# Kernel tuning notes

Hardware: AMD Instinct MI355X
Metric: run time of the kernel (lower is better)

## Reference

```python
import jax, jax.numpy as jnp
import numpy as np

N = 100000   # nodes
E = 600000   # edges
G = 512      # graphs in batch
EPS = 1e-5   # LayerNorm eps
IN_DIM = 60 + 2 + 12  # dyn feats*frames + dims + st embedding
H = 128


def setup_inputs() -> dict:
    key = jax.random.key(0)
    ks = jax.random.split(key, 32)
    inp = {
        "x": jax.random.normal(ks[0], (N, 60), jnp.float32),
        "xdims": jax.random.uniform(ks[1], (N, 2), jnp.float32),
        "xsttype": jax.random.randint(ks[2], (N,), 0, 256, jnp.int32),
        "edge_index": jax.random.randint(ks[3], (2, E), 0, N, jnp.int32),
        "batch": jnp.sort(jax.random.randint(ks[4], (N,), 0, G, jnp.int32)),
        "emb": jax.random.normal(ks[5], (256, 12), jnp.float32),
    }
    def lin(k, i, o):
        s = 1.0 / np.sqrt(i)
        return jax.random.uniform(k, (i, o), jnp.float32, -s, s)
    dims = [IN_DIM, H, H]
    for l in range(2):
        i, o = dims[l], dims[l + 1]
        inp[f"Wl{l}"] = lin(ks[6 + 4 * l], i, o)   # lin_l: applied to aggregated neighbors
        inp[f"bl{l}"] = jnp.zeros((o,), jnp.float32)
        inp[f"Wr{l}"] = lin(ks[7 + 4 * l], i, o)   # lin_r: applied to root (no bias, PyG SAGEConv)
        inp[f"g{l}"] = jnp.ones((o,), jnp.float32)   # LayerNorm gamma
        inp[f"bn{l}"] = jnp.zeros((o,), jnp.float32)  # LayerNorm beta
    ld = [2 * H, 50, 50, 10]
    for l in range(3):
        inp[f"Wf{l}"] = lin(ks[20 + l], ld[l], ld[l + 1])
        inp[f"bf{l}"] = jnp.zeros((ld[l + 1],), jnp.float32)
    return inp


def _layer_norm(h, g, b):
    mu = jnp.mean(h, axis=-1, keepdims=True)
    var = jnp.mean(jnp.square(h - mu), axis=-1, keepdims=True)
    return (h - mu) * jax.lax.rsqrt(var + EPS) * g + b


def reference(x, xdims, xsttype, edge_index, batch, emb,
              Wl0, bl0, Wr0, g0, bn0,
              Wl1, bl1, Wr1, g1, bn1,
              Wf0, bf0, Wf1, bf1, Wf2, bf2):
    # node feature assembly: [N, 60+2+12]
    h = jnp.concatenate([x, xdims, emb[xsttype]], axis=1)

    src, dst = edge_index[0], edge_index[1]
    deg = jax.ops.segment_sum(jnp.ones((E,), h.dtype), dst, num_segments=N)
    inv_deg = (1.0 / jnp.maximum(deg, 1.0))[:, None]

    for Wl, bl, Wr, g, bn in ((Wl0, bl0, Wr0, g0, bn0), (Wl1, bl1, Wr1, g1, bn1)):
        # SAGEConv (mean aggr): out = lin_l(mean_j x_j) + lin_r(x_i)
        agg = jax.ops.segment_sum(h[src], dst, num_segments=N) * inv_deg
        h = agg @ Wl + bl + h @ Wr
        h = jax.nn.relu(_layer_norm(h, g, bn))  # dropout inactive (eval)

    # global mean / max pooling over graphs
    cnt = jax.ops.segment_sum(jnp.ones((N,), h.dtype), batch, num_segments=G)
    xmean = jax.ops.segment_sum(h, batch, num_segments=G) / jnp.maximum(cnt, 1.0)[:, None]
    xmax = jax.ops.segment_max(h, batch, num_segments=G)
    z = jnp.concatenate([xmean, xmax], axis=1)  # [G, 2H]

    for Wf, bf in ((Wf0, bf0), (Wf1, bf1), (Wf2, bf2)):
        z = jax.nn.relu(z @ Wf + bf)  # Linear + ReLU + Dropout(eval)
    return z
```

## Files before the change

kernel.cpp:

```cpp
#include <hip/hip_runtime.h>

#define NN 100000
#define NP 100096
#define NT (NP / 32)
#define EE 600000
#define GG 512
#define LN_EPS 1e-5f

typedef __attribute__((ext_vector_type(8))) __bf16 bf16x8;
typedef __attribute__((ext_vector_type(4))) float f32x4;

__device__ __forceinline__ unsigned short f2bf(float f) {
    unsigned int u = __float_as_uint(f);
    u = (u + 0x7fffu + ((u >> 16) & 1u)) >> 16;
    return (unsigned short)u;
}
__device__ __forceinline__ unsigned int pack2(float a, float b) {
    return (unsigned int)f2bf(a) | ((unsigned int)f2bf(b) << 16);
}
__device__ __forceinline__ void acc8(float* s, uint4 v) {
    s[0] += __uint_as_float(v.x << 16);
    s[1] += __uint_as_float(v.x & 0xffff0000u);
    s[2] += __uint_as_float(v.y << 16);
    s[3] += __uint_as_float(v.y & 0xffff0000u);
    s[4] += __uint_as_float(v.z << 16);
    s[5] += __uint_as_float(v.z & 0xffff0000u);
    s[6] += __uint_as_float(v.w << 16);
    s[7] += __uint_as_float(v.w & 0xffff0000u);
}

#define PREP_A (NP * 10)
#define PREP_W0 (128 * 160)
#define PREP_W1 (128 * 256)
#define PREP_TOT (PREP_A + PREP_W0 + PREP_W1 + EE)

__global__ __launch_bounds__(256) void prep_kernel(
    const float* __restrict__ x, const float* __restrict__ xdims,
    const int* __restrict__ stt, const float* __restrict__ emb,
    const int* __restrict__ ei,
    const float* __restrict__ Wl0, const float* __restrict__ Wr0,
    const float* __restrict__ Wl1, const float* __restrict__ Wr1,
    unsigned short* __restrict__ H0r,
    unsigned short* __restrict__ Wt0, unsigned short* __restrict__ Wt1,
    int* __restrict__ deg)
{
    int idx = blockIdx.x * 256 + threadIdx.x;
    if (idx < PREP_A) {
        int node = idx / 10;
        int c8 = (idx - node * 10) * 8;
        unsigned short vals[8];
        if (node < NN) {
            int st = stt[node];
            #pragma unroll
            for (int i = 0; i < 8; ++i) {
                int f = c8 + i;
                float v = 0.f;
                if (f < 60)      v = x[node * 60 + f];
                else if (f < 62) v = xdims[node * 2 + (f - 60)];
                else if (f < 74) v = emb[st * 12 + (f - 62)];
                vals[i] = f2bf(v);
            }
        } else {
            #pragma unroll
            for (int i = 0; i < 8; ++i) vals[i] = 0;
        }
        uint4 o;
        o.x = (unsigned)vals[0] | ((unsigned)vals[1] << 16);
        o.y = (unsigned)vals[2] | ((unsigned)vals[3] << 16);
        o.z = (unsigned)vals[4] | ((unsigned)vals[5] << 16);
        o.w = (unsigned)vals[6] | ((unsigned)vals[7] << 16);
        *(uint4*)(H0r + (size_t)node * 80 + c8) = o;
    } else if (idx < PREP_A + PREP_W0) {
        int j = idx - PREP_A;
        int n = j / 160, k = j - n * 160;
        float v = 0.f;
        if (k < 74)                  v = Wl0[k * 128 + n];
        else if (k >= 80 && k < 154) v = Wr0[(k - 80) * 128 + n];
        Wt0[(size_t)n * 160 + k] = f2bf(v);
    } else if (idx < PREP_A + PREP_W0 + PREP_W1) {
        int j = idx - PREP_A - PREP_W0;
        int n = j >> 8, k = j & 255;
        float v = (k < 128) ? Wl1[k * 128 + n] : Wr1[(k - 128) * 128 + n];
        Wt1[(size_t)n * 256 + k] = f2bf(v);
    } else if (idx < PREP_TOT) {
        int e = idx - PREP_A - PREP_W0 - PREP_W1;
        atomicAdd(&deg[ei[EE + e]], 1);
    }
}

__global__ __launch_bounds__(256) void scan1_kernel(
    const int* __restrict__ deg, int* __restrict__ offs, int* __restrict__ bsum)
{
    __shared__ int ts[256];
    int t = threadIdx.x;
    int base = blockIdx.x * 2048 + t * 8;
    int d[8];
    if (base + 8 <= NN) {
        int4 a = *(const int4*)&deg[base];
        int4 b = *(const int4*)&deg[base + 4];
        d[0]=a.x; d[1]=a.y; d[2]=a.z; d[3]=a.w;
        d[4]=b.x; d[5]=b.y; d[6]=b.z; d[7]=b.w;
    } else {
        #pragma unroll
        for (int i = 0; i < 8; ++i) d[i] = (base + i < NN) ? deg[base + i] : 0;
    }
    int e[8]; int run = 0;
    #pragma unroll
    for (int i = 0; i < 8; ++i) { e[i] = run; run += d[i]; }
    ts[t] = run;
    int tot = run;
    __syncthreads();
    for (int off = 1; off < 256; off <<= 1) {
        int u = (t >= off) ? ts[t - off] : 0;
        __syncthreads();
        ts[t] += u;
        __syncthreads();
    }
    int pre = ts[t] - tot;
    #pragma unroll
    for (int i = 0; i < 8; ++i) if (base + i < NN) offs[base + i] = e[i] + pre;
    if (t == 255) bsum[blockIdx.x] = ts[255];
}

__global__ void scan2_kernel(int* __restrict__ bsum, int nb)
{
    int t = threadIdx.x;
    int v = (t < nb) ? bsum[t] : 0;
    int inc = v;
    for (int off = 1; off < 64; off <<= 1) {
        int u = __shfl_up(inc, off, 64);
        if (t >= off) inc += u;
    }
    if (t < nb) bsum[t] = inc - v;
}

__global__ __launch_bounds__(256) void fill_csr_kernel(
    const int* __restrict__ ei, int* __restrict__ cur,
    const int* __restrict__ offs, const int* __restrict__ bsum,
    int* __restrict__ csr)
{
    int e = blockIdx.x * 256 + threadIdx.x;
    if (e >= EE) return;
    int d = ei[EE + e];
    int p = offs[d] + bsum[d >> 11] + atomicAdd(&cur[d], 1);
    csr[p] = ei[e];
}

template<int K, bool POOL>
__global__ __launch_bounds__(256, 4) void gemm_kernel(
    const unsigned short* __restrict__ Hr,
    const unsigned short* __restrict__ Wt,
    const float* __restrict__ bias, const float* __restrict__ gamma,
    const float* __restrict__ beta,
    unsigned short* __restrict__ outH,
    const int* __restrict__ batch,
    float* __restrict__ psum, int* __restrict__ pmax, int* __restrict__ gcnt,
    const int* __restrict__ csr, const int* __restrict__ offs,
    const int* __restrict__ bsum, const int* __restrict__ deg)
{
    constexpr int KT = K / 32, AS = K + 8, KH = K / 2, CH = KH / 8;
    constexpr int SMEM = (32 * AS * 2 > 32 * 128 * 4) ? 32 * AS * 2 : 32 * 128 * 4;
    __shared__ __align__(16) char smem[SMEM];
    unsigned short* Asm = (unsigned short*)smem;
    float* Hs = (float*)smem;
    __shared__ __align__(16) float sP[32 * 4];
    __shared__ __align__(16) float qP[32 * 4];
    __shared__ int bS[POOL ? 32 : 1];

    const int tid = threadIdx.x;
    const int n0 = blockIdx.x * 32;
    const int l = tid & 63, w = tid >> 6;
    const int fg = l >> 4, c0 = l & 15;

    if (POOL && tid < 32) {
        int gn = n0 + tid;
        bS[tid] = (gn < NN) ? batch[gn] : -1;
    }
    float bia[2], gam[2], bet[2];
    #pragma unroll
    for (int j = 0; j < 2; ++j) {
        int col = (2 * w + j) * 16 + c0;
        bia[j] = bias[col]; gam[j] = gamma[col]; bet[j] = beta[col];
    }
    const unsigned short* bp0 = Wt + (size_t)((2 * w + 0) * 16 + c0) * K + fg * 8;
    const unsigned short* bp1 = Wt + (size_t)((2 * w + 1) * 16 + c0) * K + fg * 8;

    {
        const int ln = tid & 15, nl = tid >> 4;
        #pragma unroll
        for (int half = 0; half < 2; ++half) {
            int node = half * 16 + nl;
            int gn = n0 + node;
            if (ln < CH) {
                uint4 rv = *(const uint4*)(Hr + (size_t)gn * KH + ln * 8);
                int d = 0, st = 0;
                if (gn < NN) { d = deg[gn]; st = offs[gn] + bsum[gn >> 11]; }
                float iv = 1.0f / (float)(d > 1 ? d : 1);
                float s[8];
                #pragma unroll
                for (int i = 0; i < 8; ++i) s[i] = 0.f;
                int e = 0;
                for (; e + 4 <= d; e += 4) {
                    int i0 = csr[st + e],     i1 = csr[st + e + 1];
                    int i2 = csr[st + e + 2], i3 = csr[st + e + 3];
                    uint4 v0 = *(const uint4*)(Hr + (size_t)i0 * KH + ln * 8);
                    uint4 v1 = *(const uint4*)(Hr + (size_t)i1 * KH + ln * 8);
                    uint4 v2 = *(const uint4*)(Hr + (size_t)i2 * KH + ln * 8);
                    uint4 v3 = *(const uint4*)(Hr + (size_t)i3 * KH + ln * 8);
                    acc8(s, v0); acc8(s, v1); acc8(s, v2); acc8(s, v3);
                }
                for (; e < d; ++e) {
                    int i0 = csr[st + e];
                    uint4 v0 = *(const uint4*)(Hr + (size_t)i0 * KH + ln * 8);
                    acc8(s, v0);
                }
                uint4 o;
                o.x = pack2(s[0] * iv, s[1] * iv);
                o.y = pack2(s[2] * iv, s[3] * iv);
                o.z = pack2(s[4] * iv, s[5] * iv);
                o.w = pack2(s[6] * iv, s[7] * iv);
                *(uint4*)(Asm + node * AS + ln * 8) = o;
                *(uint4*)(Asm + node * AS + KH + ln * 8) = rv;
            }
        }
    }

    const unsigned short* ar0 = Asm + (0 * 16 + c0) * AS + fg * 8;
    const unsigned short* ar1 = Asm + (1 * 16 + c0) * AS + fg * 8;
    __syncthreads();

    f32x4 acc[2][2];
    acc[0][0] = (f32x4){0.f,0.f,0.f,0.f}; acc[0][1] = (f32x4){0.f,0.f,0.f,0.f};
    acc[1][0] = (f32x4){0.f,0.f,0.f,0.f}; acc[1][1] = (f32x4){0.f,0.f,0.f,0.f};

    #pragma unroll
    for (int kt = 0; kt < KT; ++kt) {
        bf16x8 b0 = *(const bf16x8*)(bp0 + kt * 32);
        bf16x8 b1 = *(const bf16x8*)(bp1 + kt * 32);
        bf16x8 a0 = *(const bf16x8*)(ar0 + kt * 32);
        bf16x8 a1 = *(const bf16x8*)(ar1 + kt * 32);
        acc[0][0] = __builtin_amdgcn_mfma_f32_16x16x32_bf16(a0, b0, acc[0][0], 0, 0, 0);
        acc[0][1] = __builtin_amdgcn_mfma_f32_16x16x32_bf16(a0, b1, acc[0][1], 0, 0, 0);
        acc[1][0] = __builtin_amdgcn_mfma_f32_16x16x32_bf16(a1, b0, acc[1][0], 0, 0, 0);
        acc[1][1] = __builtin_amdgcn_mfma_f32_16x16x32_bf16(a1, b1, acc[1][1], 0, 0, 0);
    }

    #pragma unroll
    for (int m = 0; m < 2; ++m) {
        #pragma unroll
        for (int r = 0; r < 4; ++r) {
            float h0v = acc[m][0][r] + bia[0];
            float h1v = acc[m][1][r] + bia[1];
            float s = h0v + h1v, q = h0v * h0v + h1v * h1v;
            #pragma unroll
            for (int mm = 1; mm < 16; mm <<= 1) {
                s += __shfl_xor(s, mm, 64);
                q += __shfl_xor(q, mm, 64);
            }
            if (c0 == 0) {
                int node = m * 16 + fg * 4 + r;
                sP[node * 4 + w] = s;
                qP[node * 4 + w] = q;
            }
        }
    }
    __syncthreads();

    #pragma unroll
    for (int m = 0; m < 2; ++m) {
        #pragma unroll
        for (int r = 0; r < 4; ++r) {
            int node = m * 16 + fg * 4 + r;
            float4 sv = *(const float4*)&sP[node * 4];
            float4 qv = *(const float4*)&qP[node * 4];
            float s = (sv.x + sv.y) + (sv.z + sv.w);
            float q = (qv.x + qv.y) + (qv.z + qv.w);
            float mu   = s * (1.f / 128.f);
            float var  = q * (1.f / 128.f) - mu * mu;
            float rinv = rsqrtf(var + LN_EPS);
            float h0v = acc[m][0][r] + bia[0];
            float h1v = acc[m][1][r] + bia[1];
            float v0 = fmaxf(0.f, (h0v - mu) * rinv * gam[0] + bet[0]);
            float v1 = fmaxf(0.f, (h1v - mu) * rinv * gam[1] + bet[1]);
            if (POOL) {
                Hs[node * 128 + (2 * w) * 16 + c0]     = v0;
                Hs[node * 128 + (2 * w + 1) * 16 + c0] = v1;
            } else {
                size_t gn = (size_t)(n0 + node);
                outH[gn * 128 + (2 * w) * 16 + c0]     = f2bf(v0);
                outH[gn * 128 + (2 * w + 1) * 16 + c0] = f2bf(v1);
            }
        }
    }
    if (!POOL) return;
    __syncthreads();

    if (tid < 128) {
        int j = tid;
        int curg = -1; float s = 0.f, m = 0.f; int rl = 0;
        #pragma unroll 4
        for (int n = 0; n < 32; ++n) {
            int gb = bS[n];
            if (gb < 0) break;
            if (gb != curg) {
                if (curg >= 0) {
                    atomicAdd(&psum[curg * 128 + j], s);
                    atomicMax(&pmax[curg * 128 + j], __float_as_int(m));
                    if (j == 0) atomicAdd(&gcnt[curg], rl);
                }
                curg = gb; s = 0.f; m = 0.f; rl = 0;
            }
            float v = Hs[n * 128 + j];
            s += v; m = fmaxf(m, v);
            rl += 1;
        }
        if (curg >= 0) {
            atomicAdd(&psum[curg * 128 + j], s);
            atomicMax(&pmax[curg * 128 + j], __float_as_int(m));
            if (j == 0) atomicAdd(&gcnt[curg], rl);
        }
    }
}

__global__ __launch_bounds__(64) void mlp_kernel(
    const float* __restrict__ psum, const int* __restrict__ pmax,
    const int* __restrict__ gcnt,
    const float* __restrict__ Wf0, const float* __restrict__ bf0,
    const float* __restrict__ Wf1, const float* __restrict__ bf1,
    const float* __restrict__ Wf2, const float* __restrict__ bf2,
    float* __restrict__ out)
{
    __shared__ float z[256];
    __shared__ float t1[50];
    __shared__ float t2[50];
    int g = blockIdx.x, t = threadIdx.x;
    int c = gcnt[g];
    float ic = 1.0f / (float)(c > 1 ? c : 1);
    for (int j = t; j < 128; j += 64) {
        z[j]       = psum[g * 128 + j] * ic;
        z[128 + j] = __int_as_float(pmax[g * 128 + j]);
    }
    __syncthreads();
    if (t < 50) {
        float a = bf0[t];
        for (int k = 0; k < 256; ++k) a = fmaf(z[k], Wf0[k * 50 + t], a);
        t1[t] = fmaxf(a, 0.0f);
    }
    __syncthreads();
    if (t < 50) {
        float a = bf1[t];
        for (int k = 0; k < 50; ++k) a = fmaf(t1[k], Wf1[k * 50 + t], a);
        t2[t] = fmaxf(a, 0.0f);
    }
    __syncthreads();
    if (t < 10) {
        float a = bf2[t];
        for (int k = 0; k < 50; ++k) a = fmaf(t2[k], Wf2[k * 10 + t], a);
        out[g * 10 + t] = fmaxf(a, 0.0f);
    }
}

extern "C" void kernel_launch(void* const* d_in, const int* in_sizes, int n_in,
                              void* d_out, int out_size, void* d_ws, size_t ws_size,
                              hipStream_t stream)
{
    const float* x     = (const float*)d_in[0];
    const float* xdims = (const float*)d_in[1];
    const int*   stt   = (const int*)d_in[2];
    const int*   ei    = (const int*)d_in[3];
    const int*   batch = (const int*)d_in[4];
    const float* emb   = (const float*)d_in[5];
    const float* Wl0   = (const float*)d_in[6];
    const float* bl0   = (const float*)d_in[7];
    const float* Wr0   = (const float*)d_in[8];
    const float* g0    = (const float*)d_in[9];
    const float* bn0   = (const float*)d_in[10];
    const float* Wl1   = (const float*)d_in[11];
    const float* bl1   = (const float*)d_in[12];
    const float* Wr1   = (const float*)d_in[13];
    const float* g1    = (const float*)d_in[14];
    const float* bn1   = (const float*)d_in[15];
    const float* Wf0   = (const float*)d_in[16];
    const float* bf0   = (const float*)d_in[17];
    const float* Wf1   = (const float*)d_in[18];
    const float* bf1   = (const float*)d_in[19];
    const float* Wf2   = (const float*)d_in[20];
    const float* bf2   = (const float*)d_in[21];

    char* w = (char*)d_ws;
    unsigned short* H0r = (unsigned short*)w; w += (size_t)NP * 80 * 2;
    unsigned short* H1  = (unsigned short*)w; w += (size_t)NP * 128 * 2;
    unsigned short* Wt0 = (unsigned short*)w; w += (size_t)128 * 160 * 2;
    unsigned short* Wt1 = (unsigned short*)w; w += (size_t)128 * 256 * 2;
    int*   csr    = (int*)w;   w += (size_t)EE * 4;
    int*   offs   = (int*)w;   w += (size_t)NN * 4;
    int*   bsum   = (int*)w;   w += 1024;
    char* zbeg = w;
    int*   deg  = (int*)w;   w += (size_t)NP * 4;
    int*   cur  = (int*)w;   w += (size_t)NN * 4;
    float* psum = (float*)w; w += (size_t)GG * 128 * 4;
    int*   pmax = (int*)w;   w += (size_t)GG * 128 * 4;
    int*   gcnt = (int*)w;   w += (size_t)GG * 4;
    size_t zsz = (size_t)(w - zbeg);

    hipMemsetAsync(zbeg, 0, zsz, stream);

    prep_kernel<<<(PREP_TOT + 255) / 256, 256, 0, stream>>>(
        x, xdims, stt, emb, ei, Wl0, Wr0, Wl1, Wr1, H0r, Wt0, Wt1, deg);

    int nb = (NN + 2047) / 2048;
    scan1_kernel<<<nb, 256, 0, stream>>>(deg, offs, bsum);
    scan2_kernel<<<1, 64, 0, stream>>>(bsum, nb);
    fill_csr_kernel<<<(EE + 255) / 256, 256, 0, stream>>>(ei, cur, offs, bsum, csr);

    gemm_kernel<160, false><<<NT, 256, 0, stream>>>(
        H0r, Wt0, bl0, g0, bn0, H1, nullptr, nullptr, nullptr, nullptr,
        csr, offs, bsum, deg);
    gemm_kernel<256, true><<<NT, 256, 0, stream>>>(
        H1, Wt1, bl1, g1, bn1, nullptr, batch, psum, pmax, gcnt,
        csr, offs, bsum, deg);

    mlp_kernel<<<GG, 64, 0, stream>>>(psum, pmax, gcnt, Wf0, bf0, Wf1, bf1, Wf2, bf2,
                                      (float*)d_out);
}
```

Baseline: 283.5 us.

## Use 512-thread blocks so each thread gathers one node and computes one column tile

The fused aggregate+GEMM+LayerNorm kernel moves from 256 to 512 threads per 32-node block. Each thread now gathers one node's neighbors instead of two, and each wave owns one 16-column tile instead of two. The LayerNorm partial sums grow to 8 waves per node, and padded rows are written as zeros in layer 1. The intent is more parallelism and memory-level concurrency in the latency-bound neighbor gather, at the cost of fewer MFMAs per wave and more cross-wave reduction. The MLP kernel also gets multiple independent accumulators to break FMA dependency chains.

```diff
diff --git a/kernel.cpp b/kernel.cpp
--- a/kernel.cpp
+++ b/kernel.cpp
@@ -147,7 +147,7 @@
 }
 
 template<int K, bool POOL>
-__global__ __launch_bounds__(256, 4) void gemm_kernel(
+__global__ __launch_bounds__(512, 2) void gemm_kernel(
     const unsigned short* __restrict__ Hr,
     const unsigned short* __restrict__ Wt,
     const float* __restrict__ bias, const float* __restrict__ gamma,
@@ -163,8 +163,8 @@
     __shared__ __align__(16) char smem[SMEM];
     unsigned short* Asm = (unsigned short*)smem;
     float* Hs = (float*)smem;
-    __shared__ __align__(16) float sP[32 * 4];
-    __shared__ __align__(16) float qP[32 * 4];
+    __shared__ __align__(16) float sP[32 * 8];
+    __shared__ __align__(16) float qP[32 * 8];
     __shared__ int bS[POOL ? 32 : 1];
 
     const int tid = threadIdx.x;
@@ -176,82 +176,69 @@
         int gn = n0 + tid;
         bS[tid] = (gn < NN) ? batch[gn] : -1;
     }
-    float bia[2], gam[2], bet[2];
-    #pragma unroll
-    for (int j = 0; j < 2; ++j) {
-        int col = (2 * w + j) * 16 + c0;
-        bia[j] = bias[col]; gam[j] = gamma[col]; bet[j] = beta[col];
-    }
-    const unsigned short* bp0 = Wt + (size_t)((2 * w + 0) * 16 + c0) * K + fg * 8;
-    const unsigned short* bp1 = Wt + (size_t)((2 * w + 1) * 16 + c0) * K + fg * 8;
 
     {
         const int ln = tid & 15, nl = tid >> 4;
-        #pragma unroll
-        for (int half = 0; half < 2; ++half) {
-            int node = half * 16 + nl;
-            int gn = n0 + node;
-            if (ln < CH) {
-                uint4 rv = *(const uint4*)(Hr + (size_t)gn * KH + ln * 8);
-                int d = 0, st = 0;
-                if (gn < NN) { d = deg[gn]; st = offs[gn] + bsum[gn >> 11]; }
-                float iv = 1.0f / (float)(d > 1 ? d : 1);
-                float s[8];
-                #pragma unroll
-                for (int i = 0; i < 8; ++i) s[i] = 0.f;
-                int e = 0;
-                for (; e + 4 <= d; e += 4) {
-                    int i0 = csr[st + e],     i1 = csr[st + e + 1];
-                    int i2 = csr[st + e + 2], i3 = csr[st + e + 3];
-                    uint4 v0 = *(const uint4*)(Hr + (size_t)i0 * KH + ln * 8);
-                    uint4 v1 = *(const uint4*)(Hr + (size_t)i1 * KH + ln * 8);
-                    uint4 v2 = *(const uint4*)(Hr + (size_t)i2 * KH + ln * 8);
-                    uint4 v3 = *(const uint4*)(Hr + (size_t)i3 * KH + ln * 8);
-                    acc8(s, v0); acc8(s, v1); acc8(s, v2); acc8(s, v3);
-                }
-                for (; e < d; ++e) {
-                    int i0 = csr[st + e];
-                    uint4 v0 = *(const uint4*)(Hr + (size_t)i0 * KH + ln * 8);
-                    acc8(s, v0);
-                }
-                uint4 o;
-                o.x = pack2(s[0] * iv, s[1] * iv);
-                o.y = pack2(s[2] * iv, s[3] * iv);
-                o.z = pack2(s[4] * iv, s[5] * iv);
-                o.w = pack2(s[6] * iv, s[7] * iv);
-                *(uint4*)(Asm + node * AS + ln * 8) = o;
-                *(uint4*)(Asm + node * AS + KH + ln * 8) = rv;
-            }
-        }
-    }
-
+        int gn = n0 + nl;
+        if (ln < CH) {
+            uint4 rv = *(const uint4*)(Hr + (size_t)gn * KH + ln * 8);
+            int d = 0, st = 0;
+            if (gn < NN) { d = deg[gn]; st = offs[gn] + bsum[gn >> 11]; }
+            float iv = 1.0f / (float)(d > 1 ? d : 1);
+            float s[8];
+            #pragma unroll
+            for (int i = 0; i < 8; ++i) s[i] = 0.f;
+            int e = 0;
+            for (; e + 4 <= d; e += 4) {
+                int i0 = csr[st + e],     i1 = csr[st + e + 1];
+                int i2 = csr[st + e + 2], i3 = csr[st + e + 3];
+                uint4 v0 = *(const uint4*)(Hr + (size_t)i0 * KH + ln * 8);
+                uint4 v1 = *(const uint4*)(Hr + (size_t)i1 * KH + ln * 8);
+                uint4 v2 = *(const uint4*)(Hr + (size_t)i2 * KH + ln * 8);
+                uint4 v3 = *(const uint4*)(Hr + (size_t)i3 * KH + ln * 8);
+                acc8(s, v0); acc8(s, v1); acc8(s, v2); acc8(s, v3);
+            }
+            for (; e < d; ++e) {
+                int i0 = csr[st + e];
+                uint4 v0 = *(const uint4*)(Hr + (size_t)i0 * KH + ln * 8);
+                acc8(s, v0);
+            }
+            uint4 o;
+            o.x = pack2(s[0] * iv, s[1] * iv);
+            o.y = pack2(s[2] * iv, s[3] * iv);
+            o.z = pack2(s[4] * iv, s[5] * iv);
+            o.w = pack2(s[6] * iv, s[7] * iv);
+            *(uint4*)(Asm + nl * AS + ln * 8) = o;
+            *(uint4*)(Asm + nl * AS + KH + ln * 8) = rv;
+        }
+    }
+
+    const int col = w * 16 + c0;
+    const unsigned short* bp = Wt + (size_t)col * K + fg * 8;
     const unsigned short* ar0 = Asm + (0 * 16 + c0) * AS + fg * 8;
     const unsigned short* ar1 = Asm + (1 * 16 + c0) * AS + fg * 8;
-    __syncthreads();
-
-    f32x4 acc[2][2];
-    acc[0][0] = (f32x4){0.f,0.f,0.f,0.f}; acc[0][1] = (f32x4){0.f,0.f,0.f,0.f};
-    acc[1][0] = (f32x4){0.f,0.f,0.f,0.f}; acc[1][1] = (f32x4){0.f,0.f,0.f,0.f};
+    float bia = bias[col], gam = gamma[col], bet = beta[col];
+    __syncthreads();
+
+    f32x4 acc[2];
+    acc[0] = (f32x4){0.f,0.f,0.f,0.f};
+    acc[1] = (f32x4){0.f,0.f,0.f,0.f};
 
     #pragma unroll
     for (int kt = 0; kt < KT; ++kt) {
-        bf16x8 b0 = *(const bf16x8*)(bp0 + kt * 32);
-        bf16x8 b1 = *(const bf16x8*)(bp1 + kt * 32);
+        bf16x8 b  = *(const bf16x8*)(bp  + kt * 32);
         bf16x8 a0 = *(const bf16x8*)(ar0 + kt * 32);
         bf16x8 a1 = *(const bf16x8*)(ar1 + kt * 32);
-        acc[0][0] = __builtin_amdgcn_mfma_f32_16x16x32_bf16(a0, b0, acc[0][0], 0, 0, 0);
-        acc[0][1] = __builtin_amdgcn_mfma_f32_16x16x32_bf16(a0, b1, acc[0][1], 0, 0, 0);
-        acc[1][0] = __builtin_amdgcn_mfma_f32_16x16x32_bf16(a1, b0, acc[1][0], 0, 0, 0);
-        acc[1][1] = __builtin_amdgcn_mfma_f32_16x16x32_bf16(a1, b1, acc[1][1], 0, 0, 0);
+        acc[0] = __builtin_amdgcn_mfma_f32_16x16x32_bf16(a0, b, acc[0], 0, 0, 0);
+        acc[1] = __builtin_amdgcn_mfma_f32_16x16x32_bf16(a1, b, acc[1], 0, 0, 0);
     }
 
     #pragma unroll
     for (int m = 0; m < 2; ++m) {
         #pragma unroll
         for (int r = 0; r < 4; ++r) {
-            float h0v = acc[m][0][r] + bia[0];
-            float h1v = acc[m][1][r] + bia[1];
-            float s = h0v + h1v, q = h0v * h0v + h1v * h1v;
+            float hv = acc[m][r] + bia;
+            float s = hv, q = hv * hv;
             #pragma unroll
             for (int mm = 1; mm < 16; mm <<= 1) {
                 s += __shfl_xor(s, mm, 64);
@@ -259,8 +246,8 @@
             }
             if (c0 == 0) {
                 int node = m * 16 + fg * 4 + r;
-                sP[node * 4 + w] = s;
-                qP[node * 4 + w] = q;
+                sP[node * 8 + w] = s;
+                qP[node * 8 + w] = q;
             }
         }
     }
@@ -271,24 +258,23 @@
         #pragma unroll
         for (int r = 0; r < 4; ++r) {
             int node = m * 16 + fg * 4 + r;
-            float4 sv = *(const float4*)&sP[node * 4];
-            float4 qv = *(const float4*)&qP[node * 4];
-            float s = (sv.x + sv.y) + (sv.z + sv.w);
-            float q = (qv.x + qv.y) + (qv.z + qv.w);
+            float4 sa = *(const float4*)&sP[node * 8];
+            float4 sb = *(const float4*)&sP[node * 8 + 4];
+            float4 qa = *(const float4*)&qP[node * 8];
+            float4 qb = *(const float4*)&qP[node * 8 + 4];
+            float s = ((sa.x + sa.y) + (sa.z + sa.w)) + ((sb.x + sb.y) + (sb.z + sb.w));
+            float q = ((qa.x + qa.y) + (qa.z + qa.w)) + ((qb.x + qb.y) + (qb.z + qb.w));
             float mu   = s * (1.f / 128.f);
             float var  = q * (1.f / 128.f) - mu * mu;
             float rinv = rsqrtf(var + LN_EPS);
-            float h0v = acc[m][0][r] + bia[0];
-            float h1v = acc[m][1][r] + bia[1];
-            float v0 = fmaxf(0.f, (h0v - mu) * rinv * gam[0] + bet[0]);
-            float v1 = fmaxf(0.f, (h1v - mu) * rinv * gam[1] + bet[1]);
+            float hv = acc[m][r] + bia;
+            float v0 = fmaxf(0.f, (hv - mu) * rinv * gam + bet);
             if (POOL) {
-                Hs[node * 128 + (2 * w) * 16 + c0]     = v0;
-                Hs[node * 128 + (2 * w + 1) * 16 + c0] = v1;
+                Hs[node * 128 + col] = v0;
             } else {
                 size_t gn = (size_t)(n0 + node);
-                outH[gn * 128 + (2 * w) * 16 + c0]     = f2bf(v0);
-                outH[gn * 128 + (2 * w + 1) * 16 + c0] = f2bf(v1);
+                float keep = (gn < (size_t)NN) ? 1.f : 0.f;
+                outH[gn * 128 + col] = f2bf(v0 * keep);
             }
         }
     }
@@ -342,21 +328,32 @@
     }
     __syncthreads();
     if (t < 50) {
-        float a = bf0[t];
-        for (int k = 0; k < 256; ++k) a = fmaf(z[k], Wf0[k * 50 + t], a);
-        t1[t] = fmaxf(a, 0.0f);
+        float a0 = bf0[t], a1 = 0.f, a2 = 0.f, a3 = 0.f;
+        for (int k = 0; k < 256; k += 4) {
+            a0 = fmaf(z[k],     Wf0[(k)     * 50 + t], a0);
+            a1 = fmaf(z[k + 1], Wf0[(k + 1) * 50 + t], a1);
+            a2 = fmaf(z[k + 2], Wf0[(k + 2) * 50 + t], a2);
+            a3 = fmaf(z[k + 3], Wf0[(k + 3) * 50 + t], a3);
+        }
+        t1[t] = fmaxf((a0 + a1) + (a2 + a3), 0.0f);
     }
     __syncthreads();
     if (t < 50) {
-        float a = bf1[t];
-        for (int k = 0; k < 50; ++k) a = fmaf(t1[k], Wf1[k * 50 + t], a);
-        t2[t] = fmaxf(a, 0.0f);
+        float a0 = bf1[t], a1 = 0.f;
+        for (int k = 0; k < 50; k += 2) {
+            a0 = fmaf(t1[k],     Wf1[(k)     * 50 + t], a0);
+            a1 = fmaf(t1[k + 1], Wf1[(k + 1) * 50 + t], a1);
+        }
+        t2[t] = fmaxf(a0 + a1, 0.0f);
     }
     __syncthreads();
     if (t < 10) {
-        float a = bf2[t];
-        for (int k = 0; k < 50; ++k) a = fmaf(t2[k], Wf2[k * 10 + t], a);
-        out[g * 10 + t] = fmaxf(a, 0.0f);
+        float a0 = bf2[t], a1 = 0.f;
+        for (int k = 0; k < 50; k += 2) {
+            a0 = fmaf(t2[k],     Wf2[(k)     * 10 + t], a0);
+            a1 = fmaf(t2[k + 1], Wf2[(k + 1) * 10 + t], a1);
+        }
+        out[g * 10 + t] = fmaxf(a0 + a1, 0.0f);
     }
 }
 
@@ -413,10 +410,10 @@
     scan2_kernel<<<1, 64, 0, stream>>>(bsum, nb);
     fill_csr_kernel<<<(EE + 255) / 256, 256, 0, stream>>>(ei, cur, offs, bsum, csr);
 
-    gemm_kernel<160, false><<<NT, 256, 0, stream>>>(
+    gemm_kernel<160, false><<<NT, 512, 0, stream>>>(
         H0r, Wt0, bl0, g0, bn0, H1, nullptr, nullptr, nullptr, nullptr,
         csr, offs, bsum, deg);
-    gemm_kernel<256, true><<<NT, 256, 0, stream>>>(
+    gemm_kernel<256, true><<<NT, 512, 0, stream>>>(
         H1, Wt1, bl1, g1, bn1, nullptr, batch, psum, pmax, gcnt,
         csr, offs, bsum, deg);
 
```

New measurement: 299.0 us. 5.5% more time.
